# Optimization experiments

Measured on AMD Instinct MI355X. Metric: run time of the kernel, lower is better.

The kernel has to match this reference:

```python
import jax, jax.numpy as jnp
import numpy as np

D = 64      # n_embd (== head_size in this module)
H = 8       # n_heads
B = 4
T = 2048    # seq len == block_size
EPS = 1e-5


def layernorm(x, g, b):
    mu = jnp.mean(x, axis=-1, keepdims=True)
    var = jnp.mean(jnp.square(x - mu), axis=-1, keepdims=True)
    return (x - mu) * jax.lax.rsqrt(var + EPS) * g + b


def setup_inputs() -> dict:
    key = jax.random.key(0)
    ks = jax.random.split(key, 16)
    s = 1.0 / np.sqrt(D)
    inp = {
        'inputs': jax.random.normal(ks[0], (B, T, D), jnp.float32),
        # per-head QKV linears: weight [H, D, D] (in, out), bias [H, D]
        'Wq': jax.random.uniform(ks[1], (H, D, D), jnp.float32, -s, s),
        'bq': jax.random.uniform(ks[2], (H, D), jnp.float32, -s, s),
        'Wk': jax.random.uniform(ks[3], (H, D, D), jnp.float32, -s, s),
        'bk': jax.random.uniform(ks[4], (H, D), jnp.float32, -s, s),
        'Wv': jax.random.uniform(ks[5], (H, D, D), jnp.float32, -s, s),
        'bv': jax.random.uniform(ks[6], (H, D), jnp.float32, -s, s),
        # projection: Linear(H*D -> D)
        'Wp': jax.random.uniform(ks[7], (H * D, D), jnp.float32, -1/np.sqrt(H*D), 1/np.sqrt(H*D)),
        'bp': jax.random.uniform(ks[8], (D,), jnp.float32, -1/np.sqrt(H*D), 1/np.sqrt(H*D)),
        # FFN: D -> 4D -> D
        'W1': jax.random.uniform(ks[9], (D, 4 * D), jnp.float32, -s, s),
        'b1': jax.random.uniform(ks[10], (4 * D,), jnp.float32, -s, s),
        'W2': jax.random.uniform(ks[11], (4 * D, D), jnp.float32, -1/np.sqrt(4*D), 1/np.sqrt(4*D)),
        'b2': jax.random.uniform(ks[12], (D,), jnp.float32, -1/np.sqrt(4*D), 1/np.sqrt(4*D)),
        'g1': jnp.ones((D,), jnp.float32), 'be1': jnp.zeros((D,), jnp.float32),
        'g2': jnp.ones((D,), jnp.float32), 'be2': jnp.zeros((D,), jnp.float32),
    }
    return inp


def reference(inputs, Wq, bq, Wk, bk, Wv, bv, Wp, bp, W1, b1, W2, b2, g1, be1, g2, be2):
    x = inputs
    # per-head full-width QKV: [H, B, T, D]
    q = jnp.einsum('btd,hde->hbte', x, Wq) + bq[:, None, None, :]
    k = jnp.einsum('btd,hde->hbte', x, Wk) + bk[:, None, None, :]
    v = jnp.einsum('btd,hde->hbte', x, Wv) + bv[:, None, None, :]
    # unscaled scores (module has no 1/sqrt(d) scaling)
    scores = jnp.einsum('hbte,hbse->hbts', q, k)  # [H, B, T, T]
    causal = jnp.tril(jnp.ones((T, T), bool))
    scores = jnp.where(causal, scores, -jnp.inf)
    attn = jax.nn.softmax(scores, axis=-1)
    out = jnp.einsum('hbts,hbse->hbte', attn, v)  # [H, B, T, D]
    # torch.cat over heads along last dim -> [B, T, H*D]
    cat = jnp.transpose(out, (1, 2, 0, 3)).reshape(B, T, H * D)
    attn_out = cat @ Wp + bp
    h1 = layernorm(x + attn_out, g1, be1)
    ffn = jax.nn.relu(h1 @ W1 + b1) @ W2 + b2
    return layernorm(h1 + ffn, g2, be2)
```

## Files before the change

kernel.cpp:

```cpp
#include <hip/hip_runtime.h>
#include <hip/hip_bf16.h>
#include <stdint.h>

#define Dd 64
#define Hh 8
#define Bb 4
#define Tt 2048
#define NT (Bb * Tt)

typedef __attribute__((ext_vector_type(4))) float f32x4;
typedef __attribute__((ext_vector_type(8))) __bf16 bf16x8;
typedef __attribute__((ext_vector_type(8))) uint16_t u16x8;
typedef __attribute__((ext_vector_type(4))) uint16_t u16x4;

__device__ __forceinline__ uint16_t f2bf_fast(float f) {
    union { __bf16 h; uint16_t u; } c; c.h = (__bf16)f; return c.u;
}
__device__ __forceinline__ uint32_t pkbf(float a, float b) {
    return (uint32_t)f2bf_fast(a) | ((uint32_t)f2bf_fast(b) << 16);
}

#define SWZ(row, k)   ((row) * 72  + ((k) ^ ((((row) >> 3) & 7) << 3)))
#define PSZ(q, k)     ((q)  * 72  + ((k) ^ ((((q)  >> 2) & 3) << 3)))
#define HSZ(q, k)     ((q)  * 264 + ((k) ^ ((((q)  >> 2) & 3) << 3)))
#define W2SWZ(col, k) ((col) * 264 + ((k) ^ ((((col) >> 3) & 7) << 3)))
#define WPSWZ(col, k) ((col) * 520 + ((k) ^ ((((col) >> 3) & 7) << 3)))

__global__ __launch_bounds__(256) void setup_kernel(
    const float* __restrict__ x,
    const float* __restrict__ Wq, const float* __restrict__ Wk,
    const float* __restrict__ Wv, const float* __restrict__ Wp,
    const float* __restrict__ W1, const float* __restrict__ W2,
    uint16_t* __restrict__ xb, uint16_t* __restrict__ WtAll,
    uint16_t* __restrict__ WptS, uint16_t* __restrict__ W1g,
    uint16_t* __restrict__ W2g)
{
    const int bid = blockIdx.x, t = threadIdx.x;
    if (bid < 256) {
        size_t base = ((size_t)bid * 256 + t) * 8;
        f32x4 a = *(const f32x4*)&x[base];
        f32x4 b = *(const f32x4*)&x[base + 4];
        u16x8 o;
#pragma unroll
        for (int j = 0; j < 4; ++j) { o[j] = f2bf_fast(a[j]); o[4 + j] = f2bf_fast(b[j]); }
        *(u16x8*)&xb[base] = o;
    } else if (bid < 280) {
        const int mh = bid - 256, m = mh / 8, h = mh % 8;
        const float* W = (m == 0) ? Wq : (m == 1) ? Wk : Wv;
        uint16_t* dst = WtAll + (size_t)mh * 4608;
#pragma unroll
        for (int p = 0; p < 4; ++p) {
            int idx = p * 256 + t;
            int k = idx >> 4, c4 = (idx & 15) * 4;
            f32x4 wv = *(const f32x4*)&W[(size_t)(h * 64 + k) * 64 + c4];
#pragma unroll
            for (int j = 0; j < 4; ++j) dst[SWZ(c4 + j, k)] = f2bf_fast(wv[j]);
        }
    } else if (bid < 288) {
        const int j = bid - 280;
#pragma unroll
        for (int p = 0; p < 16; ++p) {
            int idx = p * 256 + t;
            int col = idx & 63, k = j * 64 + (idx >> 6);
            WptS[WPSWZ(col, k)] = f2bf_fast(Wp[(size_t)k * 64 + col]);
        }
    } else if (bid < 292) {
        const int j = bid - 288;
#pragma unroll
        for (int p = 0; p < 16; ++p) {
            int e = j * 4096 + p * 256 + t;
            int col = e & 255, k = e >> 8;
            W1g[SWZ(col, k)] = f2bf_fast(W1[(size_t)k * 256 + col]);
        }
    } else {
        const int j = bid - 292;
#pragma unroll
        for (int p = 0; p < 16; ++p) {
            int e = j * 4096 + p * 256 + t;
            int col = e & 63, k = e >> 6;
            W2g[W2SWZ(col, k)] = f2bf_fast(W2[(size_t)k * 64 + col]);
        }
    }
}

__global__ __launch_bounds__(256) void qkv_kernel(
    const uint16_t* __restrict__ xb, const uint16_t* __restrict__ WtAll,
    const float* __restrict__ bq, const float* __restrict__ bk,
    const float* __restrict__ bv,
    uint16_t* __restrict__ qb, uint16_t* __restrict__ kb, uint16_t* __restrict__ vb)
{
    __shared__ uint16_t WtF[3][64 * 72];
    const int rt = blockIdx.x, h = blockIdx.y;
    const int t = threadIdx.x, lane = t & 63, w = t >> 6;
    const int l15 = lane & 15, g = lane >> 4;

#pragma unroll
    for (int m = 0; m < 3; ++m) {
        const u16x8* src = (const u16x8*)(WtAll + (size_t)(m * 8 + h) * 4608);
        u16x8* dst = (u16x8*)WtF[m];
        dst[t] = src[t];
        dst[256 + t] = src[256 + t];
        if (t < 64) dst[512 + t] = src[512 + t];
    }
    const int row = rt * 64 + w * 16 + l15;
    bf16x8 a0 = *(const bf16x8*)&xb[(size_t)row * 64 + g * 8];
    bf16x8 a1 = *(const bf16x8*)&xb[(size_t)row * 64 + 32 + g * 8];
    __syncthreads();

#pragma unroll
    for (int m = 0; m < 3; ++m) {
        const float* bias = (m == 0) ? bq : (m == 1) ? bk : bv;
        f32x4 acc[4] = {};
#pragma unroll
        for (int ct = 0; ct < 4; ++ct) {
            bf16x8 b0 = *(const bf16x8*)&WtF[m][SWZ(ct * 16 + l15, g * 8)];
            bf16x8 b1 = *(const bf16x8*)&WtF[m][SWZ(ct * 16 + l15, 32 + g * 8)];
            acc[ct] = __builtin_amdgcn_mfma_f32_16x16x32_bf16(a0, b0, acc[ct], 0, 0, 0);
            acc[ct] = __builtin_amdgcn_mfma_f32_16x16x32_bf16(a1, b1, acc[ct], 0, 0, 0);
        }
        if (m < 2) {
            uint16_t* out = (m == 0) ? qb : kb;
#pragma unroll
            for (int ct = 0; ct < 4; ++ct) {
                float bb = bias[h * 64 + ct * 16 + l15];
#pragma unroll
                for (int rr = 0; rr < 4; ++rr) {
                    int orow = rt * 64 + w * 16 + g * 4 + rr;
                    out[((size_t)h * NT + orow) * 64 + ct * 16 + l15] =
                        f2bf_fast(acc[ct][rr] + bb);
                }
            }
        } else {
            const size_t tb = ((size_t)h * NT + (size_t)rt * 64) * 64;
            const int kcol = (w >> 1) * 32 + g * 8 + (w & 1) * 4;
#pragma unroll
            for (int ct = 0; ct < 4; ++ct) {
                float bb = bias[h * 64 + ct * 16 + l15];
                u16x4 vo;
#pragma unroll
                for (int rr = 0; rr < 4; ++rr) vo[rr] = f2bf_fast(acc[ct][rr] + bb);
                *(u16x4*)&vb[tb + (size_t)(ct * 16 + l15) * 64 + kcol] = vo;
            }
        }
    }
}

__global__ __launch_bounds__(128) void attn_kernel7(
    const uint16_t* __restrict__ qb, const uint16_t* __restrict__ kb,
    const uint16_t* __restrict__ vb, uint16_t* __restrict__ cat)
{
    __shared__ uint16_t KsF[2][64 * 72];
    __shared__ uint16_t VtF[2][64 * 72];
    const int bid = blockIdx.x;
    const int lbid = (bid & 7) * 128 + (bid >> 3);
    const int pairid = lbid & 31;
    const int hb = lbid >> 5;
    const int h = hb & 7, b = hb >> 3;
    const int t = threadIdx.x, lane = t & 63, w = t >> 6;
    const int l15 = lane & 15, g = lane >> 4;
    const size_t base = ((size_t)h * NT + (size_t)b * Tt) * 64;
    const uint16_t* Qh  = qb + base;
    const uint16_t* Kh  = kb + base;
    const uint16_t* VhT = vb + base;

    for (int ph = 0; ph < 2; ++ph) {
        const int qt32 = ph ? (63 - pairid) : pairid;
        bf16x8 aq0, aq1;
        {
            int qrow = qt32 * 32 + w * 16 + l15;
            aq0 = *(const bf16x8*)&Qh[(size_t)qrow * 64 + g * 8];
            aq1 = *(const bf16x8*)&Qh[(size_t)qrow * 64 + 32 + g * 8];
        }
        f32x4 o[4] = {};
        float m_run = -INFINITY, l_run = 0.f;

        __syncthreads();
#pragma unroll
        for (int i = 0; i < 4; ++i) {
            int slot = i * 128 + t;
            int r = slot >> 3, c8 = (slot & 7) * 8;
            size_t off = (size_t)r * 64 + c8;
            u16x8 kk = *(const u16x8*)&Kh[off];
            u16x8 vv = *(const u16x8*)&VhT[off];
            *(u16x8*)&KsF[0][SWZ(r, c8)] = kk;
            *(u16x8*)&VtF[0][SWZ(r, c8)] = vv;
        }
        __syncthreads();

        const int nkv = (qt32 >> 1) + 1;
        for (int kv = 0; kv < nkv; ++kv) {
            const int cur = kv & 1;
            const bool pf = (kv + 1) < nkv;
            u16x8 pK[4], pV[4];
            if (pf) {
                const size_t poff = (size_t)(kv + 1) * 4096;
#pragma unroll
                for (int i = 0; i < 4; ++i) {
                    int slot = i * 128 + t;
                    size_t off = poff + (size_t)(slot >> 3) * 64 + (slot & 7) * 8;
                    pK[i] = *(const u16x8*)&Kh[off];
                    pV[i] = *(const u16x8*)&VhT[off];
                }
            }
            f32x4 s[4];
#pragma unroll
            for (int kt = 0; kt < 4; ++kt) {
                bf16x8 bk0 = *(const bf16x8*)&KsF[cur][SWZ(kt * 16 + l15, g * 8)];
                bf16x8 bk1 = *(const bf16x8*)&KsF[cur][SWZ(kt * 16 + l15, 32 + g * 8)];
                f32x4 z = {};
                z = __builtin_amdgcn_mfma_f32_16x16x32_bf16(bk0, aq0, z, 0, 0, 0);
                z = __builtin_amdgcn_mfma_f32_16x16x32_bf16(bk1, aq1, z, 0, 0, 0);
                s[kt] = z;
            }
            if (kv == nkv - 1) {
                int qlocal = (qt32 & 1) * 32 + w * 16 + l15;
#pragma unroll
                for (int kt = 0; kt < 4; ++kt)
#pragma unroll
                    for (int rj = 0; rj < 4; ++rj)
                        if (kt * 16 + g * 4 + rj > qlocal) s[kt][rj] = -INFINITY;
            }
            float mt = fmaxf(fmaxf(fmaxf(s[0][0], s[0][1]), fmaxf(s[0][2], s[0][3])),
                             fmaxf(fmaxf(s[1][0], s[1][1]), fmaxf(s[1][2], s[1][3])));
            mt = fmaxf(mt, fmaxf(fmaxf(fmaxf(s[2][0], s[2][1]), fmaxf(s[2][2], s[2][3])),
                                 fmaxf(fmaxf(s[3][0], s[3][1]), fmaxf(s[3][2], s[3][3]))));
            mt = fmaxf(mt, __shfl_xor(mt, 16));
            mt = fmaxf(mt, __shfl_xor(mt, 32));
            if (__any((int)(mt > m_run + 8.f))) {
                float mnew = fmaxf(m_run, mt);
                float alpha = __expf(m_run - mnew);
                m_run = mnew;
                l_run *= alpha;
                float a0 = __shfl(alpha, g * 4 + 0);
                float a1 = __shfl(alpha, g * 4 + 1);
                float a2 = __shfl(alpha, g * 4 + 2);
                float a3 = __shfl(alpha, g * 4 + 3);
#pragma unroll
                for (int dt = 0; dt < 4; ++dt) {
                    o[dt][0] *= a0; o[dt][1] *= a1; o[dt][2] *= a2; o[dt][3] *= a3;
                }
            }
            float ls = 0.f;
#pragma unroll
            for (int kt = 0; kt < 4; ++kt)
#pragma unroll
                for (int rj = 0; rj < 4; ++rj) {
                    float p = __expf(s[kt][rj] - m_run);
                    s[kt][rj] = p;
                    ls += p;
                }
            ls += __shfl_xor(ls, 16);
            ls += __shfl_xor(ls, 32);
            l_run += ls;
            union { uint32_t wd[4]; bf16x8 v; } ap0, ap1;
            ap0.wd[0] = pkbf(s[0][0], s[0][1]); ap0.wd[1] = pkbf(s[0][2], s[0][3]);
            ap0.wd[2] = pkbf(s[1][0], s[1][1]); ap0.wd[3] = pkbf(s[1][2], s[1][3]);
            ap1.wd[0] = pkbf(s[2][0], s[2][1]); ap1.wd[1] = pkbf(s[2][2], s[2][3]);
            ap1.wd[2] = pkbf(s[3][0], s[3][1]); ap1.wd[3] = pkbf(s[3][2], s[3][3]);
#pragma unroll
            for (int c = 0; c < 2; ++c) {
                const bf16x8 ap = c ? ap1.v : ap0.v;
#pragma unroll
                for (int dt = 0; dt < 4; ++dt) {
                    bf16x8 bv = *(const bf16x8*)&VtF[cur][SWZ(dt * 16 + l15, c * 32 + g * 8)];
                    o[dt] = __builtin_amdgcn_mfma_f32_16x16x32_bf16(ap, bv, o[dt], 0, 0, 0);
                }
            }
            if (pf) {
#pragma unroll
                for (int i = 0; i < 4; ++i) {
                    int slot = i * 128 + t;
                    int r = slot >> 3, c8 = (slot & 7) * 8;
                    *(u16x8*)&KsF[cur ^ 1][SWZ(r, c8)] = pK[i];
                    *(u16x8*)&VtF[cur ^ 1][SWZ(r, c8)] = pV[i];
                }
                __syncthreads();
            }
        }
        float inv = 1.f / l_run;
        float i0 = __shfl(inv, g * 4 + 0);
        float i1 = __shfl(inv, g * 4 + 1);
        float i2 = __shfl(inv, g * 4 + 2);
        float i3 = __shfl(inv, g * 4 + 3);
#pragma unroll
        for (int dt = 0; dt < 4; ++dt) {
            int rowb = qt32 * 32 + w * 16 + g * 4;
            size_t cb = ((size_t)b * Tt + rowb) * 512 + h * 64 + dt * 16 + l15;
            cat[cb]        = f2bf_fast(o[dt][0] * i0);
            cat[cb + 512]  = f2bf_fast(o[dt][1] * i1);
            cat[cb + 1024] = f2bf_fast(o[dt][2] * i2);
            cat[cb + 1536] = f2bf_fast(o[dt][3] * i3);
        }
    }
}

__global__ __launch_bounds__(128) void tail_kernel(
    const uint16_t* __restrict__ cat, const uint16_t* __restrict__ WptS,
    const uint16_t* __restrict__ W1g, const uint16_t* __restrict__ W2g,
    const float* __restrict__ bp, const float* __restrict__ b1,
    const float* __restrict__ b2, const float* __restrict__ x,
    const float* __restrict__ g1, const float* __restrict__ be1,
    const float* __restrict__ g2, const float* __restrict__ be2,
    float* __restrict__ out)
{
    __shared__ uint16_t h1S[2][16 * 72];
    __shared__ uint16_t hidS[2][16 * 264];
    const int rt = blockIdx.x;
    const int t = threadIdx.x, lane = t & 63, w = t >> 6;
    const int l15 = lane & 15, g = lane >> 4;
    const int arow = rt * 32 + w * 16 + l15;

    f32x4 acc[4] = {};
#pragma unroll
    for (int kt = 0; kt < 16; ++kt) {
        bf16x8 a = *(const bf16x8*)&cat[(size_t)arow * 512 + kt * 32 + g * 8];
#pragma unroll
        for (int ct = 0; ct < 4; ++ct) {
            bf16x8 bfr = *(const bf16x8*)&WptS[WPSWZ(ct * 16 + l15, kt * 32 + g * 8)];
            acc[ct] = __builtin_amdgcn_mfma_f32_16x16x32_bf16(a, bfr, acc[ct], 0, 0, 0);
        }
    }
    float bpv[4], g1v[4], b1v[4];
#pragma unroll
    for (int ct = 0; ct < 4; ++ct) {
        bpv[ct] = bp[ct * 16 + l15];
        g1v[ct] = g1[ct * 16 + l15];
        b1v[ct] = be1[ct * 16 + l15];
    }
    float hv[4][4];
#pragma unroll
    for (int rr = 0; rr < 4; ++rr) {
        int drow = rt * 32 + w * 16 + g * 4 + rr;
        float s[4], sum = 0.f;
#pragma unroll
        for (int ct = 0; ct < 4; ++ct) {
            s[ct] = acc[ct][rr] + bpv[ct] + x[(size_t)drow * 64 + ct * 16 + l15];
            sum += s[ct];
        }
        sum += __shfl_xor(sum, 1); sum += __shfl_xor(sum, 2);
        sum += __shfl_xor(sum, 4); sum += __shfl_xor(sum, 8);
        float mu = sum * (1.f / 64.f);
        float v = 0.f;
#pragma unroll
        for (int ct = 0; ct < 4; ++ct) { s[ct] -= mu; v += s[ct] * s[ct]; }
        v += __shfl_xor(v, 1); v += __shfl_xor(v, 2);
        v += __shfl_xor(v, 4); v += __shfl_xor(v, 8);
        float rstd = rsqrtf(v * (1.f / 64.f) + 1e-5f);
#pragma unroll
        for (int ct = 0; ct < 4; ++ct) {
            float h = s[ct] * rstd * g1v[ct] + b1v[ct];
            hv[ct][rr] = h;
            h1S[w][PSZ(g * 4 + rr, ct * 16 + l15)] = f2bf_fast(h);
        }
    }
    bf16x8 ha0 = *(const bf16x8*)&h1S[w][PSZ(l15, g * 8)];
    bf16x8 ha1 = *(const bf16x8*)&h1S[w][PSZ(l15, 32 + g * 8)];
#pragma unroll
    for (int nt = 0; nt < 16; ++nt) {
        f32x4 a1c = {};
        bf16x8 w10 = *(const bf16x8*)&W1g[SWZ(nt * 16 + l15, g * 8)];
        bf16x8 w11 = *(const bf16x8*)&W1g[SWZ(nt * 16 + l15, 32 + g * 8)];
        a1c = __builtin_amdgcn_mfma_f32_16x16x32_bf16(ha0, w10, a1c, 0, 0, 0);
        a1c = __builtin_amdgcn_mfma_f32_16x16x32_bf16(ha1, w11, a1c, 0, 0, 0);
        float bb1 = b1[nt * 16 + l15];
#pragma unroll
        for (int rr = 0; rr < 4; ++rr)
            hidS[w][HSZ(g * 4 + rr, nt * 16 + l15)] =
                f2bf_fast(fmaxf(a1c[rr] + bb1, 0.f));
    }
    f32x4 acc2[4] = {};
#pragma unroll
    for (int ks = 0; ks < 8; ++ks) {
        bf16x8 hfr = *(const bf16x8*)&hidS[w][HSZ(l15, ks * 32 + g * 8)];
#pragma unroll
        for (int ct = 0; ct < 4; ++ct) {
            bf16x8 w2f = *(const bf16x8*)&W2g[W2SWZ(ct * 16 + l15, ks * 32 + g * 8)];
            acc2[ct] = __builtin_amdgcn_mfma_f32_16x16x32_bf16(hfr, w2f, acc2[ct], 0, 0, 0);
        }
    }
    float b2v[4], g2v[4], be2v[4];
#pragma unroll
    for (int ct = 0; ct < 4; ++ct) {
        b2v[ct]  = b2[ct * 16 + l15];
        g2v[ct]  = g2[ct * 16 + l15];
        be2v[ct] = be2[ct * 16 + l15];
    }
#pragma unroll
    for (int rr = 0; rr < 4; ++rr) {
        int drow = rt * 32 + w * 16 + g * 4 + rr;
        float s[4], sum = 0.f;
#pragma unroll
        for (int ct = 0; ct < 4; ++ct) {
            s[ct] = acc2[ct][rr] + b2v[ct] + hv[ct][rr];
            sum += s[ct];
        }
        sum += __shfl_xor(sum, 1); sum += __shfl_xor(sum, 2);
        sum += __shfl_xor(sum, 4); sum += __shfl_xor(sum, 8);
        float mu = sum * (1.f / 64.f);
        float v = 0.f;
#pragma unroll
        for (int ct = 0; ct < 4; ++ct) { s[ct] -= mu; v += s[ct] * s[ct]; }
        v += __shfl_xor(v, 1); v += __shfl_xor(v, 2);
        v += __shfl_xor(v, 4); v += __shfl_xor(v, 8);
        float rstd = rsqrtf(v * (1.f / 64.f) + 1e-5f);
#pragma unroll
        for (int ct = 0; ct < 4; ++ct)
            out[(size_t)drow * 64 + ct * 16 + l15] =
                s[ct] * rstd * g2v[ct] + be2v[ct];
    }
}

extern "C" void kernel_launch(void* const* d_in, const int* in_sizes, int n_in,
                              void* d_out, int out_size, void* d_ws, size_t ws_size,
                              hipStream_t stream)
{
    (void)in_sizes; (void)n_in; (void)out_size; (void)ws_size;
    const float* x   = (const float*)d_in[0];
    const float* Wq  = (const float*)d_in[1];
    const float* bq  = (const float*)d_in[2];
    const float* Wk  = (const float*)d_in[3];
    const float* bk  = (const float*)d_in[4];
    const float* Wv  = (const float*)d_in[5];
    const float* bv  = (const float*)d_in[6];
    const float* Wp  = (const float*)d_in[7];
    const float* bp  = (const float*)d_in[8];
    const float* W1  = (const float*)d_in[9];
    const float* b1  = (const float*)d_in[10];
    const float* W2  = (const float*)d_in[11];
    const float* b2  = (const float*)d_in[12];
    const float* g1  = (const float*)d_in[13];
    const float* be1 = (const float*)d_in[14];
    const float* g2  = (const float*)d_in[15];
    const float* be2 = (const float*)d_in[16];
    float* outp = (float*)d_out;

    char* w = (char*)d_ws;
    uint16_t* qb   = (uint16_t*)w;
    uint16_t* kb   = qb + (size_t)Hh * NT * 64;
    uint16_t* vb   = kb + (size_t)Hh * NT * 64;
    uint16_t* cat  = vb + (size_t)Hh * NT * 64;
    uint16_t* WptS = cat + (size_t)NT * 512;
    uint16_t* W1g  = WptS + 33280;
    uint16_t* W2g  = W1g + 18432;
    uint16_t* xb   = W2g + 16896;
    uint16_t* WtAll= xb + (size_t)NT * 64;

    setup_kernel<<<dim3(296), dim3(256), 0, stream>>>(
        x, Wq, Wk, Wv, Wp, W1, W2, xb, WtAll, WptS, W1g, W2g);
    qkv_kernel<<<dim3(NT / 64, Hh), dim3(256), 0, stream>>>(
        xb, WtAll, bq, bk, bv, qb, kb, vb);
    attn_kernel7<<<dim3(1024), dim3(128), 0, stream>>>(qb, kb, vb, cat);
    tail_kernel<<<dim3(256), dim3(128), 0, stream>>>(
        cat, WptS, W1g, W2g, bp, b1, b2, x, g1, be1, g2, be2, outp);
}
```

Baseline: 165.2 us.

## Fold log2e into Q, use exp2, MFMA row sums, 64-row query tiles

```diff
diff --git a/kernel.cpp b/kernel.cpp
--- a/kernel.cpp
+++ b/kernel.cpp
@@ -25,6 +25,8 @@
 #define HSZ(q, k)     ((q)  * 264 + ((k) ^ ((((q)  >> 2) & 3) << 3)))
 #define W2SWZ(col, k) ((col) * 264 + ((k) ^ ((((col) >> 3) & 7) << 3)))
 #define WPSWZ(col, k) ((col) * 520 + ((k) ^ ((((col) >> 3) & 7) << 3)))
+
+#define LOG2E 1.44269504f
 
 __global__ __launch_bounds__(256) void setup_kernel(
     const float* __restrict__ x,
@@ -120,6 +122,7 @@
         }
         if (m < 2) {
             uint16_t* out = (m == 0) ? qb : kb;
+            const float scl = (m == 0) ? LOG2E : 1.0f;
 #pragma unroll
             for (int ct = 0; ct < 4; ++ct) {
                 float bb = bias[h * 64 + ct * 16 + l15];
@@ -127,7 +130,7 @@
                 for (int rr = 0; rr < 4; ++rr) {
                     int orow = rt * 64 + w * 16 + g * 4 + rr;
                     out[((size_t)h * NT + orow) * 64 + ct * 16 + l15] =
-                        f2bf_fast(acc[ct][rr] + bb);
+                        f2bf_fast((acc[ct][rr] + bb) * scl);
                 }
             }
         } else {
@@ -145,16 +148,16 @@
     }
 }
 
-__global__ __launch_bounds__(128) void attn_kernel7(
+__global__ __launch_bounds__(256) void attn_kernel8(
     const uint16_t* __restrict__ qb, const uint16_t* __restrict__ kb,
     const uint16_t* __restrict__ vb, uint16_t* __restrict__ cat)
 {
     __shared__ uint16_t KsF[2][64 * 72];
     __shared__ uint16_t VtF[2][64 * 72];
     const int bid = blockIdx.x;
-    const int lbid = (bid & 7) * 128 + (bid >> 3);
-    const int pairid = lbid & 31;
-    const int hb = lbid >> 5;
+    const int lbid = (bid & 7) * 64 + (bid >> 3);
+    const int pairid = lbid & 15;
+    const int hb = lbid >> 4;
     const int h = hb & 7, b = hb >> 3;
     const int t = threadIdx.x, lane = t & 63, w = t >> 6;
     const int l15 = lane & 15, g = lane >> 4;
@@ -163,21 +166,27 @@
     const uint16_t* Kh  = kb + base;
     const uint16_t* VhT = vb + base;
 
+    union { uint32_t u[4]; bf16x8 v; } onesu;
+#pragma unroll
+    for (int j = 0; j < 4; ++j) onesu.u[j] = 0x3F803F80u;
+    const bf16x8 ones = onesu.v;
+
     for (int ph = 0; ph < 2; ++ph) {
-        const int qt32 = ph ? (63 - pairid) : pairid;
+        const int qt = ph ? (31 - pairid) : pairid;
         bf16x8 aq0, aq1;
         {
-            int qrow = qt32 * 32 + w * 16 + l15;
+            int qrow = qt * 64 + w * 16 + l15;
             aq0 = *(const bf16x8*)&Qh[(size_t)qrow * 64 + g * 8];
             aq1 = *(const bf16x8*)&Qh[(size_t)qrow * 64 + 32 + g * 8];
         }
         f32x4 o[4] = {};
-        float m_run = -INFINITY, l_run = 0.f;
+        f32x4 l_acc = {};
+        float m_run = -INFINITY;
 
         __syncthreads();
 #pragma unroll
-        for (int i = 0; i < 4; ++i) {
-            int slot = i * 128 + t;
+        for (int i = 0; i < 2; ++i) {
+            int slot = i * 256 + t;
             int r = slot >> 3, c8 = (slot & 7) * 8;
             size_t off = (size_t)r * 64 + c8;
             u16x8 kk = *(const u16x8*)&Kh[off];
@@ -187,16 +196,16 @@
         }
         __syncthreads();
 
-        const int nkv = (qt32 >> 1) + 1;
+        const int nkv = qt + 1;
         for (int kv = 0; kv < nkv; ++kv) {
             const int cur = kv & 1;
             const bool pf = (kv + 1) < nkv;
-            u16x8 pK[4], pV[4];
+            u16x8 pK[2], pV[2];
             if (pf) {
                 const size_t poff = (size_t)(kv + 1) * 4096;
 #pragma unroll
-                for (int i = 0; i < 4; ++i) {
-                    int slot = i * 128 + t;
+                for (int i = 0; i < 2; ++i) {
+                    int slot = i * 256 + t;
                     size_t off = poff + (size_t)(slot >> 3) * 64 + (slot & 7) * 8;
                     pK[i] = *(const u16x8*)&Kh[off];
                     pV[i] = *(const u16x8*)&VhT[off];
@@ -213,7 +222,7 @@
                 s[kt] = z;
             }
             if (kv == nkv - 1) {
-                int qlocal = (qt32 & 1) * 32 + w * 16 + l15;
+                int qlocal = w * 16 + l15;
 #pragma unroll
                 for (int kt = 0; kt < 4; ++kt)
 #pragma unroll
@@ -226,32 +235,25 @@
                                  fmaxf(fmaxf(s[3][0], s[3][1]), fmaxf(s[3][2], s[3][3]))));
             mt = fmaxf(mt, __shfl_xor(mt, 16));
             mt = fmaxf(mt, __shfl_xor(mt, 32));
-            if (__any((int)(mt > m_run + 8.f))) {
+            if (__any((int)(mt > m_run + 11.5409f))) {
                 float mnew = fmaxf(m_run, mt);
-                float alpha = __expf(m_run - mnew);
+                float alpha = exp2f(m_run - mnew);
                 m_run = mnew;
-                l_run *= alpha;
                 float a0 = __shfl(alpha, g * 4 + 0);
                 float a1 = __shfl(alpha, g * 4 + 1);
                 float a2 = __shfl(alpha, g * 4 + 2);
                 float a3 = __shfl(alpha, g * 4 + 3);
+                l_acc[0] *= a0; l_acc[1] *= a1; l_acc[2] *= a2; l_acc[3] *= a3;
 #pragma unroll
                 for (int dt = 0; dt < 4; ++dt) {
                     o[dt][0] *= a0; o[dt][1] *= a1; o[dt][2] *= a2; o[dt][3] *= a3;
                 }
             }
-            float ls = 0.f;
 #pragma unroll
             for (int kt = 0; kt < 4; ++kt)
 #pragma unroll
-                for (int rj = 0; rj < 4; ++rj) {
-                    float p = __expf(s[kt][rj] - m_run);
-                    s[kt][rj] = p;
-                    ls += p;
-                }
-            ls += __shfl_xor(ls, 16);
-            ls += __shfl_xor(ls, 32);
-            l_run += ls;
+                for (int rj = 0; rj < 4; ++rj)
+                    s[kt][rj] = exp2f(s[kt][rj] - m_run);
             union { uint32_t wd[4]; bf16x8 v; } ap0, ap1;
             ap0.wd[0] = pkbf(s[0][0], s[0][1]); ap0.wd[1] = pkbf(s[0][2], s[0][3]);
             ap0.wd[2] = pkbf(s[1][0], s[1][1]); ap0.wd[3] = pkbf(s[1][2], s[1][3]);
@@ -260,6 +262,7 @@
 #pragma unroll
             for (int c = 0; c < 2; ++c) {
                 const bf16x8 ap = c ? ap1.v : ap0.v;
+                l_acc = __builtin_amdgcn_mfma_f32_16x16x32_bf16(ap, ones, l_acc, 0, 0, 0);
 #pragma unroll
                 for (int dt = 0; dt < 4; ++dt) {
                     bf16x8 bv = *(const bf16x8*)&VtF[cur][SWZ(dt * 16 + l15, c * 32 + g * 8)];
@@ -268,8 +271,8 @@
             }
             if (pf) {
 #pragma unroll
-                for (int i = 0; i < 4; ++i) {
-                    int slot = i * 128 + t;
+                for (int i = 0; i < 2; ++i) {
+                    int slot = i * 256 + t;
                     int r = slot >> 3, c8 = (slot & 7) * 8;
                     *(u16x8*)&KsF[cur ^ 1][SWZ(r, c8)] = pK[i];
                     *(u16x8*)&VtF[cur ^ 1][SWZ(r, c8)] = pV[i];
@@ -277,19 +280,17 @@
                 __syncthreads();
             }
         }
-        float inv = 1.f / l_run;
-        float i0 = __shfl(inv, g * 4 + 0);
-        float i1 = __shfl(inv, g * 4 + 1);
-        float i2 = __shfl(inv, g * 4 + 2);
-        float i3 = __shfl(inv, g * 4 + 3);
+        f32x4 inv;
+#pragma unroll
+        for (int rj = 0; rj < 4; ++rj) inv[rj] = 1.f / l_acc[rj];
 #pragma unroll
         for (int dt = 0; dt < 4; ++dt) {
-            int rowb = qt32 * 32 + w * 16 + g * 4;
+            int rowb = qt * 64 + w * 16 + g * 4;
             size_t cb = ((size_t)b * Tt + rowb) * 512 + h * 64 + dt * 16 + l15;
-            cat[cb]        = f2bf_fast(o[dt][0] * i0);
-            cat[cb + 512]  = f2bf_fast(o[dt][1] * i1);
-            cat[cb + 1024] = f2bf_fast(o[dt][2] * i2);
-            cat[cb + 1536] = f2bf_fast(o[dt][3] * i3);
+            cat[cb]        = f2bf_fast(o[dt][0] * inv[0]);
+            cat[cb + 512]  = f2bf_fast(o[dt][1] * inv[1]);
+            cat[cb + 1024] = f2bf_fast(o[dt][2] * inv[2]);
+            cat[cb + 1536] = f2bf_fast(o[dt][3] * inv[3]);
         }
     }
 }
@@ -449,7 +450,7 @@
         x, Wq, Wk, Wv, Wp, W1, W2, xb, WtAll, WptS, W1g, W2g);
     qkv_kernel<<<dim3(NT / 64, Hh), dim3(256), 0, stream>>>(
         xb, WtAll, bq, bk, bv, qb, kb, vb);
-    attn_kernel7<<<dim3(1024), dim3(128), 0, stream>>>(qb, kb, vb, cat);
+    attn_kernel8<<<dim3(512), dim3(256), 0, stream>>>(qb, kb, vb, cat);
     tail_kernel<<<dim3(256), dim3(128), 0, stream>>>(
         cat, WptS, W1g, W2g, bp, b1, b2, x, g1, be1, g2, be2, outp);
 }
```

Measured after the change: 162.6 us. No clear change (-1.6%).
